# Kernel tuning notes

Measured on AMD Instinct MI355X. Metric: run time of the kernel, lower is better.

Reference implementation:

```python
import jax, jax.numpy as jnp
import numpy as np

N_NODES = 100000
N_EDGES = 300000
D = 256
N_LAYERS = 4
BN_EPS = 1e-5


def setup_inputs() -> dict:
    key = jax.random.key(0)
    ks = jax.random.split(key, 6)
    x = jax.random.normal(ks[0], (N_NODES, D), dtype=jnp.float32)
    rows = jax.random.randint(ks[1], (N_EDGES,), 0, N_NODES)
    cols = jax.random.randint(ks[2], (N_EDGES,), 0, N_NODES)
    vals = jax.random.uniform(ks[3], (N_EDGES,), dtype=jnp.float32)
    stdv = 1.0 / np.sqrt(D).astype(np.float32)
    weights = jax.random.uniform(ks[4], (N_LAYERS, D, D), jnp.float32, -stdv, stdv)
    self_weights = jax.random.uniform(ks[5], (N_LAYERS, D, D), jnp.float32, -stdv, stdv)
    gammas = jnp.ones((N_LAYERS, D), jnp.float32)
    betas = jnp.zeros((N_LAYERS, D), jnp.float32)
    return {"x": x, "vals": vals, "weights": weights, "self_weights": self_weights,
            "gammas": gammas, "betas": betas, "rows": rows, "cols": cols}


def reference(x, vals, weights, self_weights, gammas, betas, rows, cols):
    n = x.shape[0]

    def gcn_layer(h, W, SW, gamma, beta):
        # support = h @ W  -> dense [N, D]
        support = h @ W
        # spmm(adj, support): out[i] = sum_{e: rows[e]==i} vals[e] * support[cols[e]]
        agg = jax.ops.segment_sum(vals[:, None] * support[cols], rows, num_segments=n)
        out = agg + h @ SW  # self-loop term (withloop=True)
        # BatchNorm1d over nodes (training-mode batch stats, biased variance)
        mean = out.mean(axis=0)
        var = out.var(axis=0)
        out = gamma * (out - mean) * jax.lax.rsqrt(var + BN_EPS) + beta
        return jax.nn.relu(out)

    h = x
    for i in range(N_LAYERS):
        h = gcn_layer(h, weights[i], self_weights[i], gammas[i], betas[i])
    # aggrmethod='concat', dense=False -> cat(final, input)
    return jnp.concatenate([h, x], axis=1)
```

## Files before the change

### kernel.cpp

```cpp
#include <hip/hip_runtime.h>
#include <hip/hip_bf16.h>
#include <stdint.h>

#define M_NODES 100000
#define NE      300000
#define D       256
#define D2      512
#define NLAYERS 4

typedef float  f32x4  __attribute__((ext_vector_type(4)));
typedef __bf16 bf16x8 __attribute__((ext_vector_type(8)));

static __device__ __forceinline__ float bf2f(uint32_t u) {
  union { uint32_t i; float f; } v; v.i = u << 16; return v.f;
}
static __device__ __forceinline__ uint32_t f2bf(float f) {
  union { float f; uint32_t i; } v; v.f = f;
  return (v.i + 0x7fffu + ((v.i >> 16) & 1u)) >> 16;
}
static __device__ __forceinline__ void gload_lds16(const void* g, void* l) {
  __builtin_amdgcn_global_load_lds((const __attribute__((address_space(1))) uint32_t*)g,
                                   (__attribute__((address_space(3))) uint32_t*)l, 16, 0, 0);
}

__global__ void hist_kernel(const int* __restrict__ rows, int* __restrict__ counts) {
  int e = blockIdx.x * 256 + threadIdx.x;
  if (e < NE) atomicAdd(&counts[rows[e]], 1);
}

__global__ void scan1_kernel(const int* __restrict__ counts, int* __restrict__ rp,
                             int* __restrict__ bsum) {
  __shared__ int sd[256];
  int tid = threadIdx.x;
  int base = blockIdx.x * 1024 + tid * 4;
  int v0 = (base + 0 < M_NODES) ? counts[base + 0] : 0;
  int v1 = (base + 1 < M_NODES) ? counts[base + 1] : 0;
  int v2 = (base + 2 < M_NODES) ? counts[base + 2] : 0;
  int v3 = (base + 3 < M_NODES) ? counts[base + 3] : 0;
  int tsum = v0 + v1 + v2 + v3;
  sd[tid] = tsum; __syncthreads();
  for (int off = 1; off < 256; off <<= 1) {
    int x = sd[tid];
    if (tid >= off) x += sd[tid - off];
    __syncthreads(); sd[tid] = x; __syncthreads();
  }
  int excl = sd[tid] - tsum;
  if (base + 0 < M_NODES) rp[base + 0] = excl; excl += v0;
  if (base + 1 < M_NODES) rp[base + 1] = excl; excl += v1;
  if (base + 2 < M_NODES) rp[base + 2] = excl; excl += v2;
  if (base + 3 < M_NODES) rp[base + 3] = excl;
  if (tid == 255) bsum[blockIdx.x] = sd[255];
}

__global__ void scan2_kernel(const int* __restrict__ bsum, int* __restrict__ boff) {
  __shared__ int sd[128];
  int tid = threadIdx.x;
  int v = (tid < 98) ? bsum[tid] : 0;
  sd[tid] = v; __syncthreads();
  for (int off = 1; off < 128; off <<= 1) {
    int x = sd[tid];
    if (tid >= off) x += sd[tid - off];
    __syncthreads(); sd[tid] = x; __syncthreads();
  }
  if (tid < 98) boff[tid] = sd[tid] - v;
}

__global__ void scan3_kernel(int* __restrict__ rp, const int* __restrict__ boff,
                             int* __restrict__ cursor) {
  int i = blockIdx.x * 256 + threadIdx.x;
  if (i > M_NODES) return;
  int v = (i < M_NODES) ? rp[i] + boff[i >> 10] : NE;
  rp[i] = v;
  if (i < M_NODES) cursor[i] = v;
}

__global__ void scatter_kernel(const int* __restrict__ rows, const int* __restrict__ cols,
                               const float* __restrict__ vals, int* __restrict__ cursor,
                               int* __restrict__ e_col, float* __restrict__ e_val) {
  int e = blockIdx.x * 256 + threadIdx.x;
  if (e >= NE) return;
  int r = rows[e];
  int p = atomicAdd(&cursor[r], 1);
  e_col[p] = cols[e];
  e_val[p] = vals[e];
}

__global__ void prep_x_kernel(const float* __restrict__ x, ushort* __restrict__ h,
                              float* __restrict__ out) {
  size_t idx = (size_t)blockIdx.x * 256 + threadIdx.x;
  size_t i = idx >> 6; int c = (int)(idx & 63) * 4;
  float4 v = *(const float4*)(x + i * D + c);
  *(float4*)(out + i * D2 + D + c) = v;
  ushort4 o;
  o.x = (ushort)f2bf(v.x); o.y = (ushort)f2bf(v.y);
  o.z = (ushort)f2bf(v.z); o.w = (ushort)f2bf(v.w);
  *(ushort4*)(h + i * D + c) = o;
}

__global__ void conv_w_kernel(const float* __restrict__ W, const float* __restrict__ SW,
                              ushort* __restrict__ Bt) {
  int idx = blockIdx.x * 256 + threadIdx.x;
  if (idx >= NLAYERS * D2 * D) return;
  int k = idx & (D - 1);
  int n = (idx >> 8) & (D2 - 1);
  int layer = idx >> 17;
  float v = (n < D) ? W[(size_t)layer * D * D + k * D + n]
                    : SW[(size_t)layer * D * D + k * D + (n - D)];
  Bt[idx] = (ushort)f2bf(v);
}

#define BM 128
#define BN 128
#define BK 64

__global__ __launch_bounds__(256, 2)
void gemm_kernel(const ushort* __restrict__ h, const ushort* __restrict__ Bt,
                 ushort* __restrict__ outAB) {
  __shared__ __align__(16) ushort As[BM * BK];
  __shared__ __align__(16) ushort Bs[BN * BK];
  const int tid = threadIdx.x;
  const int m0 = blockIdx.x * BM;
  const int n0 = blockIdx.y * BN;
  const int wv = tid >> 6, l = tid & 63;
  const int wr = wv >> 1, wc = wv & 1;
  const int lrow = l & 15, lhi = l >> 4;

  f32x4 acc[4][4] = {};

  const int arow = tid >> 3;
  const int acb  = (tid & 7) << 4;

#pragma unroll
  for (int s = 0; s < 4; ++s) {
    const int k0 = s * BK;
#pragma unroll
    for (int p = 0; p < 4; ++p) {
      int row = p * 32 + arow;
      int grow = m0 + row; if (grow >= M_NODES) grow = M_NODES - 1;
      int gcb = acb ^ ((row & 7) << 4);
      gload_lds16(h + (size_t)grow * D + k0 + (gcb >> 1), As + row * BK + (acb >> 1));
    }
#pragma unroll
    for (int p = 0; p < 4; ++p) {
      int row = p * 32 + arow;
      int gn = n0 + row;
      int gcb = acb ^ ((row & 7) << 4);
      gload_lds16(Bt + (size_t)gn * D + k0 + (gcb >> 1), Bs + row * BK + (acb >> 1));
    }
    __syncthreads();
#pragma unroll
    for (int kk = 0; kk < 2; ++kk) {
      bf16x8 af[4], bfr[4];
#pragma unroll
      for (int mi = 0; mi < 4; ++mi) {
        int row = wr * 64 + mi * 16 + lrow;
        int off = row * 128 + ((kk * 64 + lhi * 16) ^ ((row & 7) << 4));
        af[mi] = *(const bf16x8*)((const char*)As + off);
      }
#pragma unroll
      for (int nj = 0; nj < 4; ++nj) {
        int row = wc * 64 + nj * 16 + lrow;
        int off = row * 128 + ((kk * 64 + lhi * 16) ^ ((row & 7) << 4));
        bfr[nj] = *(const bf16x8*)((const char*)Bs + off);
      }
#pragma unroll
      for (int mi = 0; mi < 4; ++mi)
#pragma unroll
        for (int nj = 0; nj < 4; ++nj)
          acc[mi][nj] = __builtin_amdgcn_mfma_f32_16x16x32_bf16(af[mi], bfr[nj], acc[mi][nj], 0, 0, 0);
    }
    __syncthreads();
  }

#pragma unroll
  for (int mi = 0; mi < 4; ++mi) {
#pragma unroll
    for (int nj = 0; nj < 4; ++nj) {
      int gc = n0 + wc * 64 + nj * 16 + lrow;
#pragma unroll
      for (int r = 0; r < 4; ++r) {
        int grow = m0 + wr * 64 + mi * 16 + lhi * 4 + r;
        if (grow < M_NODES)
          outAB[(size_t)grow * D2 + gc] = (ushort)f2bf(acc[mi][nj][r]);
      }
    }
  }
}

#define SPMM_CHUNK 16

__global__ __launch_bounds__(256, 4)
void spmm_kernel(ushort* __restrict__ AB, const int* __restrict__ rp,
                 const int* __restrict__ e_col, const float* __restrict__ e_val,
                 float* __restrict__ stats) {
  __shared__ float sstats[2 * D];
  for (int i = threadIdx.x; i < 2 * D; i += 256) sstats[i] = 0.f;
  __syncthreads();

  const int wv = threadIdx.x >> 6, l = threadIdx.x & 63;
  const int hl = l >> 5, lc = l & 31;
  const int wave = blockIdx.x * 4 + wv;
  const int row0 = wave * SPMM_CHUNK;

  float s[8] = {}, q[8] = {};

  if (row0 < M_NODES) {
    int myrp = (l <= SPMM_CHUNK) ? rp[row0 + l] : 0;
    const int ebase = __shfl(myrp, 0);
    const int ecnt  = __shfl(myrp, SPMM_CHUNK) - ebase;
    int   myc0 = (l < ecnt)      ? e_col[ebase + l]      : 0;
    float myv0 = (l < ecnt)      ? e_val[ebase + l]      : 0.f;
    int   myc1 = (64 + l < ecnt) ? e_col[ebase + 64 + l] : 0;
    float myv1 = (64 + l < ecnt) ? e_val[ebase + 64 + l] : 0.f;

    for (int t = 0; t < SPMM_CHUNK; t += 2) {
      const int i = row0 + t + hl;
      const int eA0 = __shfl(myrp, t);
      const int eA1 = __shfl(myrp, t + 1);
      const int eB1 = __shfl(myrp, t + 2);
      const int d0 = eA1 - eA0, d1 = eB1 - eA1;
      const int e0  = hl ? eA1 : eA0;
      const int deg = hl ? d1  : d0;
      const int degmax = (d0 > d1) ? d0 : d1;

      float a[8] = {};

      for (int b = 0; b < degmax; b += 4) {
        float vv[4]; uint4 sp[4];
#pragma unroll
        for (int j = 0; j < 4; ++j) {
          int ej = b + j;
          int ecl = (ej < deg) ? ej : ((deg > 0) ? deg - 1 : 0);
          int slot = e0 - ebase + ecl;
          int sl = slot & 63;
          int cA = __shfl(myc0, sl);
          int cB = __shfl(myc1, sl);
          float vA = __shfl(myv0, sl);
          float vB = __shfl(myv1, sl);
          int   c = (slot < 64) ? cA : cB;
          float v = (slot < 64) ? vA : vB;
          if (slot >= 128 && ej < deg) {
            c = e_col[e0 + ecl]; v = e_val[e0 + ecl];
          }
          vv[j] = (ej < deg) ? v : 0.f;
          sp[j] = *(const uint4*)(AB + (size_t)c * D2 + lc * 8);
        }
#pragma unroll
        for (int j = 0; j < 4; ++j) {
          a[0] += vv[j] * bf2f(sp[j].x & 0xffff);
          a[1] += vv[j] * bf2f(sp[j].x >> 16);
          a[2] += vv[j] * bf2f(sp[j].y & 0xffff);
          a[3] += vv[j] * bf2f(sp[j].y >> 16);
          a[4] += vv[j] * bf2f(sp[j].z & 0xffff);
          a[5] += vv[j] * bf2f(sp[j].z >> 16);
          a[6] += vv[j] * bf2f(sp[j].w & 0xffff);
          a[7] += vv[j] * bf2f(sp[j].w >> 16);
        }
      }

      const uint4 st = *(const uint4*)(AB + (size_t)i * D2 + D + lc * 8);
      a[0] += bf2f(st.x & 0xffff); a[1] += bf2f(st.x >> 16);
      a[2] += bf2f(st.y & 0xffff); a[3] += bf2f(st.y >> 16);
      a[4] += bf2f(st.z & 0xffff); a[5] += bf2f(st.z >> 16);
      a[6] += bf2f(st.w & 0xffff); a[7] += bf2f(st.w >> 16);

      uint4 o;
      o.x = f2bf(a[0]) | (f2bf(a[1]) << 16);
      o.y = f2bf(a[2]) | (f2bf(a[3]) << 16);
      o.z = f2bf(a[4]) | (f2bf(a[5]) << 16);
      o.w = f2bf(a[6]) | (f2bf(a[7]) << 16);
      *(uint4*)(AB + (size_t)i * D2 + D + lc * 8) = o;

#pragma unroll
      for (int k = 0; k < 8; ++k) { s[k] += a[k]; q[k] += a[k] * a[k]; }
    }
  }

  const int c0 = lc * 8;
#pragma unroll
  for (int k = 0; k < 8; ++k) {
    atomicAdd(&sstats[c0 + k], s[k]);
    atomicAdd(&sstats[D + c0 + k], q[k]);
  }
  __syncthreads();
  atomicAdd(&stats[threadIdx.x], sstats[threadIdx.x]);
  atomicAdd(&stats[D + threadIdx.x], sstats[D + threadIdx.x]);
}

template<bool LAST>
__global__ void norm_kernel(const ushort* __restrict__ AB, const float* __restrict__ stats,
                            const float* __restrict__ gamma, const float* __restrict__ beta,
                            ushort* __restrict__ hout, float* __restrict__ out) {
  const int cs = threadIdx.x & 31;
  const int rr = threadIdx.x >> 5;
  const int c0 = cs * 8;

  float sc[8], sh[8];
#pragma unroll
  for (int k = 0; k < 8; ++k) {
    float mean = stats[c0 + k] * (1.0f / M_NODES);
    float var  = stats[D + c0 + k] * (1.0f / M_NODES) - mean * mean;
    float rstd = rsqrtf(var + 1e-5f);
    float g = gamma[c0 + k];
    sc[k] = g * rstd;
    sh[k] = beta[c0 + k] - mean * sc[k];
  }

  const int r0 = blockIdx.x * 64;
#pragma unroll
  for (int rb = 0; rb < 8; ++rb) {
    int r = r0 + rb * 8 + rr;
    if (r >= M_NODES) break;
    const uint4 u = *(const uint4*)(AB + (size_t)r * D2 + D + c0);
    float f[8];
    f[0] = bf2f(u.x & 0xffff); f[1] = bf2f(u.x >> 16);
    f[2] = bf2f(u.y & 0xffff); f[3] = bf2f(u.y >> 16);
    f[4] = bf2f(u.z & 0xffff); f[5] = bf2f(u.z >> 16);
    f[6] = bf2f(u.w & 0xffff); f[7] = bf2f(u.w >> 16);
#pragma unroll
    for (int k = 0; k < 8; ++k) f[k] = fmaxf(f[k] * sc[k] + sh[k], 0.f);
    if (LAST) {
      float4 r0v = { f[0], f[1], f[2], f[3] };
      float4 r1v = { f[4], f[5], f[6], f[7] };
      *(float4*)(out + (size_t)r * D2 + c0) = r0v;
      *(float4*)(out + (size_t)r * D2 + c0 + 4) = r1v;
    } else {
      uint4 o;
      o.x = f2bf(f[0]) | (f2bf(f[1]) << 16);
      o.y = f2bf(f[2]) | (f2bf(f[3]) << 16);
      o.z = f2bf(f[4]) | (f2bf(f[5]) << 16);
      o.w = f2bf(f[6]) | (f2bf(f[7]) << 16);
      *(uint4*)(hout + (size_t)r * D + c0) = o;
    }
  }
}

extern "C" void kernel_launch(void* const* d_in, const int* in_sizes, int n_in,
                              void* d_out, int out_size, void* d_ws, size_t ws_size,
                              hipStream_t stream) {
  const float* x      = (const float*)d_in[0];
  const float* vals   = (const float*)d_in[1];
  const float* W      = (const float*)d_in[2];
  const float* SW     = (const float*)d_in[3];
  const float* gammas = (const float*)d_in[4];
  const float* betas  = (const float*)d_in[5];
  const int*   rows   = (const int*)d_in[6];
  const int*   cols   = (const int*)d_in[7];
  float* out = (float*)d_out;

  char* ws = (char*)d_ws;
  size_t off = 0;
  auto alloc = [&](size_t bytes) {
    void* p = ws + off;
    off = (off + bytes + 255) & ~(size_t)255;
    return p;
  };
  ushort* h    = (ushort*)alloc((size_t)M_NODES * D * 2);
  ushort* AB   = (ushort*)alloc((size_t)M_NODES * D2 * 2);
  ushort* Bt   = (ushort*)alloc((size_t)NLAYERS * D2 * D * 2);
  int*   rp    = (int*)alloc((M_NODES + 1) * 4);
  int*   cursor= (int*)alloc((M_NODES + 1) * 4);
  int*   e_col = (int*)alloc(NE * 4);
  float* e_val = (float*)alloc(NE * 4);
  int*   bsum  = (int*)alloc(512);
  int*   boff  = (int*)alloc(512);
  float* stats = (float*)alloc(NLAYERS * 2 * D * 4);

  hipMemsetAsync(cursor, 0, (size_t)M_NODES * 4, stream);
  hipMemsetAsync(stats, 0, (size_t)NLAYERS * 2 * D * 4, stream);

  hist_kernel<<<(NE + 255) / 256, 256, 0, stream>>>(rows, cursor);
  scan1_kernel<<<98, 256, 0, stream>>>(cursor, rp, bsum);
  scan2_kernel<<<1, 128, 0, stream>>>(bsum, boff);
  scan3_kernel<<<(M_NODES + 256) / 256, 256, 0, stream>>>(rp, boff, cursor);
  scatter_kernel<<<(NE + 255) / 256, 256, 0, stream>>>(rows, cols, vals, cursor, e_col, e_val);

  prep_x_kernel<<<(M_NODES * D / 4) / 256, 256, 0, stream>>>(x, h, out);
  conv_w_kernel<<<(NLAYERS * D2 * D) / 256, 256, 0, stream>>>(W, SW, Bt);

  const int spmm_blocks = (M_NODES + SPMM_CHUNK * 4 - 1) / (SPMM_CHUNK * 4);
  const int norm_blocks = (M_NODES + 63) / 64;
  for (int lyr = 0; lyr < NLAYERS; ++lyr) {
    gemm_kernel<<<dim3((M_NODES + BM - 1) / BM, D2 / BN), 256, 0, stream>>>(
        h, Bt + (size_t)lyr * D2 * D, AB);
    spmm_kernel<<<spmm_blocks, 256, 0, stream>>>(AB, rp, e_col, e_val,
                                                 stats + (size_t)lyr * 2 * D);
    if (lyr < NLAYERS - 1)
      norm_kernel<false><<<norm_blocks, 256, 0, stream>>>(
          AB, stats + (size_t)lyr * 2 * D, gammas + lyr * D, betas + lyr * D, h, nullptr);
    else
      norm_kernel<true><<<norm_blocks, 256, 0, stream>>>(
          AB, stats + (size_t)lyr * 2 * D, gammas + lyr * D, betas + lyr * D, nullptr, out);
  }
}
```

Before: 717.5 us.

## Stage SpMM edge metadata in LDS, widen gather unroll, two-stage stats reduction

Each wave now stages up to 256 edges' column/value pairs in shared memory instead of holding them in registers and broadcasting with shuffles; edges beyond 256 fall back to global loads. The neighbor-gather loop is unrolled to 8 loads in flight instead of 4. Per-block BN statistics are written to a partial buffer and summed by a separate small reduce kernel rather than with global atomics. The changes aim to cut shuffle overhead, raise memory-level parallelism and remove atomic contention, at the cost of extra LDS use (possibly lower occupancy), one more kernel launch per layer and more wasted gather lanes on low-degree rows.

```diff
diff --git a/kernel.cpp b/kernel.cpp
--- a/kernel.cpp
+++ b/kernel.cpp
@@ -7,6 +7,9 @@
 #define D       256
 #define D2      512
 #define NLAYERS 4
+
+#define SPMM_CHUNK  16
+#define SPMM_BLOCKS ((M_NODES + SPMM_CHUNK * 4 - 1) / (SPMM_CHUNK * 4))
 
 typedef float  f32x4  __attribute__((ext_vector_type(4)));
 typedef __bf16 bf16x8 __attribute__((ext_vector_type(8)));
@@ -187,32 +190,38 @@
   }
 }
 
-#define SPMM_CHUNK 16
-
 __global__ __launch_bounds__(256, 4)
 void spmm_kernel(ushort* __restrict__ AB, const int* __restrict__ rp,
                  const int* __restrict__ e_col, const float* __restrict__ e_val,
-                 float* __restrict__ stats) {
+                 float* __restrict__ partial) {
   __shared__ float sstats[2 * D];
+  __shared__ uint2 emeta[4][256];
   for (int i = threadIdx.x; i < 2 * D; i += 256) sstats[i] = 0.f;
-  __syncthreads();
 
   const int wv = threadIdx.x >> 6, l = threadIdx.x & 63;
   const int hl = l >> 5, lc = l & 31;
-  const int wave = blockIdx.x * 4 + wv;
-  const int row0 = wave * SPMM_CHUNK;
+  const int row0 = (blockIdx.x * 4 + wv) * SPMM_CHUNK;
+  const bool active = row0 < M_NODES;
+
+  int myrp = 0, ebase = 0, ecnt = 0;
+  if (active) {
+    myrp = (l <= SPMM_CHUNK) ? rp[row0 + l] : 0;
+    ebase = __shfl(myrp, 0);
+    ecnt  = __shfl(myrp, SPMM_CHUNK) - ebase;
+    for (int e = l; e < 256; e += 64) {
+      uint2 m = {0u, 0u};
+      if (e < ecnt) {
+        m.x = (uint32_t)e_col[ebase + e];
+        m.y = __float_as_uint(e_val[ebase + e]);
+      }
+      emeta[wv][e] = m;
+    }
+  }
+  __syncthreads();
 
   float s[8] = {}, q[8] = {};
 
-  if (row0 < M_NODES) {
-    int myrp = (l <= SPMM_CHUNK) ? rp[row0 + l] : 0;
-    const int ebase = __shfl(myrp, 0);
-    const int ecnt  = __shfl(myrp, SPMM_CHUNK) - ebase;
-    int   myc0 = (l < ecnt)      ? e_col[ebase + l]      : 0;
-    float myv0 = (l < ecnt)      ? e_val[ebase + l]      : 0.f;
-    int   myc1 = (64 + l < ecnt) ? e_col[ebase + 64 + l] : 0;
-    float myv1 = (64 + l < ecnt) ? e_val[ebase + 64 + l] : 0.f;
-
+  if (active) {
     for (int t = 0; t < SPMM_CHUNK; t += 2) {
       const int i = row0 + t + hl;
       const int eA0 = __shfl(myrp, t);
@@ -225,28 +234,25 @@
 
       float a[8] = {};
 
-      for (int b = 0; b < degmax; b += 4) {
-        float vv[4]; uint4 sp[4];
-#pragma unroll
-        for (int j = 0; j < 4; ++j) {
+      for (int b = 0; b < degmax; b += 8) {
+        float vv[8]; uint4 sp[8];
+#pragma unroll
+        for (int j = 0; j < 8; ++j) {
           int ej = b + j;
           int ecl = (ej < deg) ? ej : ((deg > 0) ? deg - 1 : 0);
           int slot = e0 - ebase + ecl;
-          int sl = slot & 63;
-          int cA = __shfl(myc0, sl);
-          int cB = __shfl(myc1, sl);
-          float vA = __shfl(myv0, sl);
-          float vB = __shfl(myv1, sl);
-          int   c = (slot < 64) ? cA : cB;
-          float v = (slot < 64) ? vA : vB;
-          if (slot >= 128 && ej < deg) {
+          int c; float v;
+          if (slot < 256) {
+            uint2 m = emeta[wv][slot];
+            c = (int)m.x; v = __uint_as_float(m.y);
+          } else {
             c = e_col[e0 + ecl]; v = e_val[e0 + ecl];
           }
           vv[j] = (ej < deg) ? v : 0.f;
           sp[j] = *(const uint4*)(AB + (size_t)c * D2 + lc * 8);
         }
 #pragma unroll
-        for (int j = 0; j < 4; ++j) {
+        for (int j = 0; j < 8; ++j) {
           a[0] += vv[j] * bf2f(sp[j].x & 0xffff);
           a[1] += vv[j] * bf2f(sp[j].x >> 16);
           a[2] += vv[j] * bf2f(sp[j].y & 0xffff);
@@ -283,8 +289,20 @@
     atomicAdd(&sstats[D + c0 + k], q[k]);
   }
   __syncthreads();
-  atomicAdd(&stats[threadIdx.x], sstats[threadIdx.x]);
-  atomicAdd(&stats[D + threadIdx.x], sstats[D + threadIdx.x]);
+  partial[(size_t)blockIdx.x * 2 * D + threadIdx.x]     = sstats[threadIdx.x];
+  partial[(size_t)blockIdx.x * 2 * D + D + threadIdx.x] = sstats[D + threadIdx.x];
+}
+
+__global__ void reduce_stats_kernel(const float* __restrict__ partial,
+                                    float* __restrict__ stats) {
+  const int t = threadIdx.x;
+  float rs = 0.f, rq = 0.f;
+  for (int b = blockIdx.x; b < SPMM_BLOCKS; b += 64) {
+    rs += partial[(size_t)b * 2 * D + t];
+    rq += partial[(size_t)b * 2 * D + D + t];
+  }
+  atomicAdd(&stats[t], rs);
+  atomicAdd(&stats[D + t], rq);
 }
 
 template<bool LAST>
@@ -355,16 +373,17 @@
     off = (off + bytes + 255) & ~(size_t)255;
     return p;
   };
-  ushort* h    = (ushort*)alloc((size_t)M_NODES * D * 2);
-  ushort* AB   = (ushort*)alloc((size_t)M_NODES * D2 * 2);
-  ushort* Bt   = (ushort*)alloc((size_t)NLAYERS * D2 * D * 2);
-  int*   rp    = (int*)alloc((M_NODES + 1) * 4);
-  int*   cursor= (int*)alloc((M_NODES + 1) * 4);
-  int*   e_col = (int*)alloc(NE * 4);
-  float* e_val = (float*)alloc(NE * 4);
-  int*   bsum  = (int*)alloc(512);
-  int*   boff  = (int*)alloc(512);
-  float* stats = (float*)alloc(NLAYERS * 2 * D * 4);
+  ushort* h      = (ushort*)alloc((size_t)M_NODES * D * 2);
+  ushort* AB     = (ushort*)alloc((size_t)M_NODES * D2 * 2);
+  ushort* Bt     = (ushort*)alloc((size_t)NLAYERS * D2 * D * 2);
+  int*   rp      = (int*)alloc((M_NODES + 1) * 4);
+  int*   cursor  = (int*)alloc((M_NODES + 1) * 4);
+  int*   e_col   = (int*)alloc(NE * 4);
+  float* e_val   = (float*)alloc(NE * 4);
+  int*   bsum    = (int*)alloc(512);
+  int*   boff    = (int*)alloc(512);
+  float* stats   = (float*)alloc(NLAYERS * 2 * D * 4);
+  float* partial = (float*)alloc((size_t)SPMM_BLOCKS * 2 * D * 4);
 
   hipMemsetAsync(cursor, 0, (size_t)M_NODES * 4, stream);
   hipMemsetAsync(stats, 0, (size_t)NLAYERS * 2 * D * 4, stream);
@@ -378,13 +397,12 @@
   prep_x_kernel<<<(M_NODES * D / 4) / 256, 256, 0, stream>>>(x, h, out);
   conv_w_kernel<<<(NLAYERS * D2 * D) / 256, 256, 0, stream>>>(W, SW, Bt);
 
-  const int spmm_blocks = (M_NODES + SPMM_CHUNK * 4 - 1) / (SPMM_CHUNK * 4);
   const int norm_blocks = (M_NODES + 63) / 64;
   for (int lyr = 0; lyr < NLAYERS; ++lyr) {
     gemm_kernel<<<dim3((M_NODES + BM - 1) / BM, D2 / BN), 256, 0, stream>>>(
         h, Bt + (size_t)lyr * D2 * D, AB);
-    spmm_kernel<<<spmm_blocks, 256, 0, stream>>>(AB, rp, e_col, e_val,
-                                                 stats + (size_t)lyr * 2 * D);
+    spmm_kernel<<<SPMM_BLOCKS, 256, 0, stream>>>(AB, rp, e_col, e_val, partial);
+    reduce_stats_kernel<<<64, 256, 0, stream>>>(partial, stats + (size_t)lyr * 2 * D);
     if (lyr < NLAYERS - 1)
       norm_kernel<false><<<norm_blocks, 256, 0, stream>>>(
           AB, stats + (size_t)lyr * 2 * D, gammas + lyr * D, betas + lyr * D, h, nullptr);
```

After: 771.2 us. 1.07x slower.

## Restructure SpMM to one row pair per wave with packed edge metadata

Applied to the files above, without the earlier changes.

The SpMM kernel now gives each wave a single pair of rows, using 1024-thread blocks, instead of a 16-row chunk processed serially. This spreads the work across many more waves and exposes more parallel gather loads. Edge column and value are packed into one uint2 array, so a single 8-byte load replaces two separate loads. Column statistics are reduced across the two half-waves with a shuffle before the shared atomics. In exchange there are more blocks and more global atomics per row, and the grid assumes M_NODES divides evenly by 32.

```diff
diff --git a/kernel.cpp b/kernel.cpp
--- a/kernel.cpp
+++ b/kernel.cpp
@@ -7,6 +7,9 @@
 #define D       256
 #define D2      512
 #define NLAYERS 4
+
+#define SPMM_TPB  1024
+#define SPMM_GRID (M_NODES / (2 * (SPMM_TPB / 64)))
 
 typedef float  f32x4  __attribute__((ext_vector_type(4)));
 typedef __bf16 bf16x8 __attribute__((ext_vector_type(8)));
@@ -76,13 +79,13 @@
 
 __global__ void scatter_kernel(const int* __restrict__ rows, const int* __restrict__ cols,
                                const float* __restrict__ vals, int* __restrict__ cursor,
-                               int* __restrict__ e_col, float* __restrict__ e_val) {
+                               uint2* __restrict__ emeta) {
   int e = blockIdx.x * 256 + threadIdx.x;
   if (e >= NE) return;
   int r = rows[e];
   int p = atomicAdd(&cursor[r], 1);
-  e_col[p] = cols[e];
-  e_val[p] = vals[e];
+  uint2 m; m.x = (uint32_t)cols[e]; m.y = __float_as_uint(vals[e]);
+  emeta[p] = m;
 }
 
 __global__ void prep_x_kernel(const float* __restrict__ x, ushort* __restrict__ h,
@@ -187,104 +190,90 @@
   }
 }
 
-#define SPMM_CHUNK 16
-
-__global__ __launch_bounds__(256, 4)
+__global__ __launch_bounds__(SPMM_TPB)
 void spmm_kernel(ushort* __restrict__ AB, const int* __restrict__ rp,
-                 const int* __restrict__ e_col, const float* __restrict__ e_val,
-                 float* __restrict__ stats) {
+                 const uint2* __restrict__ emeta, float* __restrict__ stats) {
   __shared__ float sstats[2 * D];
-  for (int i = threadIdx.x; i < 2 * D; i += 256) sstats[i] = 0.f;
+  for (int i = threadIdx.x; i < 2 * D; i += SPMM_TPB) sstats[i] = 0.f;
   __syncthreads();
 
-  const int wv = threadIdx.x >> 6, l = threadIdx.x & 63;
+  const int l  = threadIdx.x & 63;
+  const int wv = threadIdx.x >> 6;
   const int hl = l >> 5, lc = l & 31;
-  const int wave = blockIdx.x * 4 + wv;
-  const int row0 = wave * SPMM_CHUNK;
-
-  float s[8] = {}, q[8] = {};
-
-  if (row0 < M_NODES) {
-    int myrp = (l <= SPMM_CHUNK) ? rp[row0 + l] : 0;
-    const int ebase = __shfl(myrp, 0);
-    const int ecnt  = __shfl(myrp, SPMM_CHUNK) - ebase;
-    int   myc0 = (l < ecnt)      ? e_col[ebase + l]      : 0;
-    float myv0 = (l < ecnt)      ? e_val[ebase + l]      : 0.f;
-    int   myc1 = (64 + l < ecnt) ? e_col[ebase + 64 + l] : 0;
-    float myv1 = (64 + l < ecnt) ? e_val[ebase + 64 + l] : 0.f;
-
-    for (int t = 0; t < SPMM_CHUNK; t += 2) {
-      const int i = row0 + t + hl;
-      const int eA0 = __shfl(myrp, t);
-      const int eA1 = __shfl(myrp, t + 1);
-      const int eB1 = __shfl(myrp, t + 2);
-      const int d0 = eA1 - eA0, d1 = eB1 - eA1;
-      const int e0  = hl ? eA1 : eA0;
-      const int deg = hl ? d1  : d0;
-      const int degmax = (d0 > d1) ? d0 : d1;
-
-      float a[8] = {};
-
-      for (int b = 0; b < degmax; b += 4) {
-        float vv[4]; uint4 sp[4];
-#pragma unroll
-        for (int j = 0; j < 4; ++j) {
-          int ej = b + j;
-          int ecl = (ej < deg) ? ej : ((deg > 0) ? deg - 1 : 0);
-          int slot = e0 - ebase + ecl;
-          int sl = slot & 63;
-          int cA = __shfl(myc0, sl);
-          int cB = __shfl(myc1, sl);
-          float vA = __shfl(myv0, sl);
-          float vB = __shfl(myv1, sl);
-          int   c = (slot < 64) ? cA : cB;
-          float v = (slot < 64) ? vA : vB;
-          if (slot >= 128 && ej < deg) {
-            c = e_col[e0 + ecl]; v = e_val[e0 + ecl];
-          }
-          vv[j] = (ej < deg) ? v : 0.f;
-          sp[j] = *(const uint4*)(AB + (size_t)c * D2 + lc * 8);
-        }
-#pragma unroll
-        for (int j = 0; j < 4; ++j) {
-          a[0] += vv[j] * bf2f(sp[j].x & 0xffff);
-          a[1] += vv[j] * bf2f(sp[j].x >> 16);
-          a[2] += vv[j] * bf2f(sp[j].y & 0xffff);
-          a[3] += vv[j] * bf2f(sp[j].y >> 16);
-          a[4] += vv[j] * bf2f(sp[j].z & 0xffff);
-          a[5] += vv[j] * bf2f(sp[j].z >> 16);
-          a[6] += vv[j] * bf2f(sp[j].w & 0xffff);
-          a[7] += vv[j] * bf2f(sp[j].w >> 16);
-        }
+  const int pair = blockIdx.x * (SPMM_TPB / 64) + wv;
+  const int row  = pair * 2 + hl;
+
+  int myrp = (l < 3) ? rp[pair * 2 + l] : 0;
+  const int lo  = __shfl(myrp, 0);
+  const int mid = __shfl(myrp, 1);
+  const int end = __shfl(myrp, 2);
+  const int ebase = lo, ecnt = end - lo;
+  const int e0  = hl ? mid : lo;
+  const int d0 = mid - lo, d1 = end - mid;
+  const int deg = hl ? d1 : d0;
+  const int degmax = (d0 > d1) ? d0 : d1;
+
+  uint2 mymeta = {0u, 0u};
+  if (l < ecnt) mymeta = emeta[ebase + l];
+
+  const uint4 st = *(const uint4*)(AB + (size_t)row * D2 + D + lc * 8);
+
+  float a[8] = {};
+  for (int b = 0; b < degmax; b += 4) {
+    float vv[4]; uint4 sp[4];
+#pragma unroll
+    for (int j = 0; j < 4; ++j) {
+      int ej = b + j;
+      int ecl = (ej < deg) ? ej : ((deg > 0) ? deg - 1 : 0);
+      int slot = e0 - ebase + ecl;
+      int sl = slot & 63;
+      int c   = __shfl((int)mymeta.x, sl);
+      float v = __shfl(__uint_as_float(mymeta.y), sl);
+      if (slot >= 64 && ej < deg) {
+        uint2 m = emeta[e0 + ecl]; c = (int)m.x; v = __uint_as_float(m.y);
       }
-
-      const uint4 st = *(const uint4*)(AB + (size_t)i * D2 + D + lc * 8);
-      a[0] += bf2f(st.x & 0xffff); a[1] += bf2f(st.x >> 16);
-      a[2] += bf2f(st.y & 0xffff); a[3] += bf2f(st.y >> 16);
-      a[4] += bf2f(st.z & 0xffff); a[5] += bf2f(st.z >> 16);
-      a[6] += bf2f(st.w & 0xffff); a[7] += bf2f(st.w >> 16);
-
-      uint4 o;
-      o.x = f2bf(a[0]) | (f2bf(a[1]) << 16);
-      o.y = f2bf(a[2]) | (f2bf(a[3]) << 16);
-      o.z = f2bf(a[4]) | (f2bf(a[5]) << 16);
-      o.w = f2bf(a[6]) | (f2bf(a[7]) << 16);
-      *(uint4*)(AB + (size_t)i * D2 + D + lc * 8) = o;
-
-#pragma unroll
-      for (int k = 0; k < 8; ++k) { s[k] += a[k]; q[k] += a[k] * a[k]; }
-    }
-  }
+      vv[j] = (ej < deg) ? v : 0.f;
+      sp[j] = *(const uint4*)(AB + (size_t)c * D2 + lc * 8);
+    }
+#pragma unroll
+    for (int j = 0; j < 4; ++j) {
+      a[0] += vv[j] * bf2f(sp[j].x & 0xffff);
+      a[1] += vv[j] * bf2f(sp[j].x >> 16);
+      a[2] += vv[j] * bf2f(sp[j].y & 0xffff);
+      a[3] += vv[j] * bf2f(sp[j].y >> 16);
+      a[4] += vv[j] * bf2f(sp[j].z & 0xffff);
+      a[5] += vv[j] * bf2f(sp[j].z >> 16);
+      a[6] += vv[j] * bf2f(sp[j].w & 0xffff);
+      a[7] += vv[j] * bf2f(sp[j].w >> 16);
+    }
+  }
+
+  a[0] += bf2f(st.x & 0xffff); a[1] += bf2f(st.x >> 16);
+  a[2] += bf2f(st.y & 0xffff); a[3] += bf2f(st.y >> 16);
+  a[4] += bf2f(st.z & 0xffff); a[5] += bf2f(st.z >> 16);
+  a[6] += bf2f(st.w & 0xffff); a[7] += bf2f(st.w >> 16);
+
+  uint4 o;
+  o.x = f2bf(a[0]) | (f2bf(a[1]) << 16);
+  o.y = f2bf(a[2]) | (f2bf(a[3]) << 16);
+  o.z = f2bf(a[4]) | (f2bf(a[5]) << 16);
+  o.w = f2bf(a[6]) | (f2bf(a[7]) << 16);
+  *(uint4*)(AB + (size_t)row * D2 + D + lc * 8) = o;
 
   const int c0 = lc * 8;
 #pragma unroll
   for (int k = 0; k < 8; ++k) {
-    atomicAdd(&sstats[c0 + k], s[k]);
-    atomicAdd(&sstats[D + c0 + k], q[k]);
+    float a2 = a[k] * a[k];
+    float sk = a[k] + __shfl_xor(a[k], 32);
+    float qk = a2   + __shfl_xor(a2,   32);
+    if (hl == 0) {
+      atomicAdd(&sstats[c0 + k], sk);
+      atomicAdd(&sstats[D + c0 + k], qk);
+    }
   }
   __syncthreads();
-  atomicAdd(&stats[threadIdx.x], sstats[threadIdx.x]);
-  atomicAdd(&stats[D + threadIdx.x], sstats[D + threadIdx.x]);
+  if (threadIdx.x < 2 * D)
+    atomicAdd(&stats[threadIdx.x], sstats[threadIdx.x]);
 }
 
 template<bool LAST>
@@ -355,16 +344,15 @@
     off = (off + bytes + 255) & ~(size_t)255;
     return p;
   };
-  ushort* h    = (ushort*)alloc((size_t)M_NODES * D * 2);
-  ushort* AB   = (ushort*)alloc((size_t)M_NODES * D2 * 2);
-  ushort* Bt   = (ushort*)alloc((size_t)NLAYERS * D2 * D * 2);
-  int*   rp    = (int*)alloc((M_NODES + 1) * 4);
-  int*   cursor= (int*)alloc((M_NODES + 1) * 4);
-  int*   e_col = (int*)alloc(NE * 4);
-  float* e_val = (float*)alloc(NE * 4);
-  int*   bsum  = (int*)alloc(512);
-  int*   boff  = (int*)alloc(512);
-  float* stats = (float*)alloc(NLAYERS * 2 * D * 4);
+  ushort* h     = (ushort*)alloc((size_t)M_NODES * D * 2);
+  ushort* AB    = (ushort*)alloc((size_t)M_NODES * D2 * 2);
+  ushort* Bt    = (ushort*)alloc((size_t)NLAYERS * D2 * D * 2);
+  int*   rp     = (int*)alloc((M_NODES + 1) * 4);
+  int*   cursor = (int*)alloc((M_NODES + 1) * 4);
+  uint2* emeta  = (uint2*)alloc((size_t)NE * 8);
+  int*   bsum   = (int*)alloc(512);
+  int*   boff   = (int*)alloc(512);
+  float* stats  = (float*)alloc(NLAYERS * 2 * D * 4);
 
   hipMemsetAsync(cursor, 0, (size_t)M_NODES * 4, stream);
   hipMemsetAsync(stats, 0, (size_t)NLAYERS * 2 * D * 4, stream);
@@ -373,18 +361,17 @@
   scan1_kernel<<<98, 256, 0, stream>>>(cursor, rp, bsum);
   scan2_kernel<<<1, 128, 0, stream>>>(bsum, boff);
   scan3_kernel<<<(M_NODES + 256) / 256, 256, 0, stream>>>(rp, boff, cursor);
-  scatter_kernel<<<(NE + 255) / 256, 256, 0, stream>>>(rows, cols, vals, cursor, e_col, e_val);
+  scatter_kernel<<<(NE + 255) / 256, 256, 0, stream>>>(rows, cols, vals, cursor, emeta);
 
   prep_x_kernel<<<(M_NODES * D / 4) / 256, 256, 0, stream>>>(x, h, out);
   conv_w_kernel<<<(NLAYERS * D2 * D) / 256, 256, 0, stream>>>(W, SW, Bt);
 
-  const int spmm_blocks = (M_NODES + SPMM_CHUNK * 4 - 1) / (SPMM_CHUNK * 4);
   const int norm_blocks = (M_NODES + 63) / 64;
   for (int lyr = 0; lyr < NLAYERS; ++lyr) {
     gemm_kernel<<<dim3((M_NODES + BM - 1) / BM, D2 / BN), 256, 0, stream>>>(
         h, Bt + (size_t)lyr * D2 * D, AB);
-    spmm_kernel<<<spmm_blocks, 256, 0, stream>>>(AB, rp, e_col, e_val,
-                                                 stats + (size_t)lyr * 2 * D);
+    spmm_kernel<<<SPMM_GRID, SPMM_TPB, 0, stream>>>(AB, rp, emeta,
+                                                    stats + (size_t)lyr * 2 * D);
     if (lyr < NLAYERS - 1)
       norm_kernel<false><<<norm_blocks, 256, 0, stream>>>(
           AB, stats + (size_t)lyr * 2 * D, gammas + lyr * D, betas + lyr * D, h, nullptr);
```

Measured after the change: 1.145 ms. 59.5% more time.

## Fuse BatchNorm+ReLU into next GEMM's A-load and restructure SpMM

Applied to the files above, without the earlier changes.

Drops the per-layer norm kernel for intermediate layers. A tiny kernel now computes the BN scale and shift, and the next GEMM applies scale, shift, ReLU and the bf16 conversion while loading A tiles through registers instead of direct global-to-LDS loads. Layer 0 converts fp32 x on the fly, which removes the bf16 copy of h. SpMM now gives one row per wave with 4 columns per lane, packs col and val into one uint2 array, writes to a separate P buffer, and raises its occupancy bound. The cost is extra ALU work and register-path loads in the GEMM prologue, and the normalize work is repeated across the four N-tile blocks.

```diff
diff --git a/kernel.cpp b/kernel.cpp
--- a/kernel.cpp
+++ b/kernel.cpp
@@ -7,6 +7,8 @@
 #define D       256
 #define D2      512
 #define NLAYERS 4
+
+#define SPMM_CHUNK 16
 
 typedef float  f32x4  __attribute__((ext_vector_type(4)));
 typedef __bf16 bf16x8 __attribute__((ext_vector_type(8)));
@@ -76,25 +78,20 @@
 
 __global__ void scatter_kernel(const int* __restrict__ rows, const int* __restrict__ cols,
                                const float* __restrict__ vals, int* __restrict__ cursor,
-                               int* __restrict__ e_col, float* __restrict__ e_val) {
+                               uint2* __restrict__ emeta) {
   int e = blockIdx.x * 256 + threadIdx.x;
   if (e >= NE) return;
   int r = rows[e];
   int p = atomicAdd(&cursor[r], 1);
-  e_col[p] = cols[e];
-  e_val[p] = vals[e];
-}
-
-__global__ void prep_x_kernel(const float* __restrict__ x, ushort* __restrict__ h,
-                              float* __restrict__ out) {
+  uint2 m; m.x = (uint32_t)cols[e]; m.y = __float_as_uint(vals[e]);
+  emeta[p] = m;
+}
+
+__global__ void prep_x_kernel(const float* __restrict__ x, float* __restrict__ out) {
   size_t idx = (size_t)blockIdx.x * 256 + threadIdx.x;
   size_t i = idx >> 6; int c = (int)(idx & 63) * 4;
   float4 v = *(const float4*)(x + i * D + c);
   *(float4*)(out + i * D2 + D + c) = v;
-  ushort4 o;
-  o.x = (ushort)f2bf(v.x); o.y = (ushort)f2bf(v.y);
-  o.z = (ushort)f2bf(v.z); o.w = (ushort)f2bf(v.w);
-  *(ushort4*)(h + i * D + c) = o;
 }
 
 __global__ void conv_w_kernel(const float* __restrict__ W, const float* __restrict__ SW,
@@ -109,12 +106,25 @@
   Bt[idx] = (ushort)f2bf(v);
 }
 
+__global__ void bn_fin_kernel(const float* __restrict__ stats, const float* __restrict__ gamma,
+                              const float* __restrict__ beta, float* __restrict__ ss) {
+  int c = threadIdx.x;
+  float mean = stats[c] * (1.0f / M_NODES);
+  float var  = stats[D + c] * (1.0f / M_NODES) - mean * mean;
+  float rstd = rsqrtf(var + 1e-5f);
+  float sc = gamma[c] * rstd;
+  ss[c] = sc;
+  ss[D + c] = beta[c] - mean * sc;
+}
+
 #define BM 128
 #define BN 128
 #define BK 64
 
+template<int MODE>
 __global__ __launch_bounds__(256, 2)
-void gemm_kernel(const ushort* __restrict__ h, const ushort* __restrict__ Bt,
+void gemm_kernel(const float* __restrict__ x, const ushort* __restrict__ P,
+                 const float* __restrict__ ss, const ushort* __restrict__ Bt,
                  ushort* __restrict__ outAB) {
   __shared__ __align__(16) ushort As[BM * BK];
   __shared__ __align__(16) ushort Bs[BN * BK];
@@ -129,16 +139,45 @@
 
   const int arow = tid >> 3;
   const int acb  = (tid & 7) << 4;
+  const int acol = acb >> 1;
 
 #pragma unroll
   for (int s = 0; s < 4; ++s) {
     const int k0 = s * BK;
+    float4 sc0, sc1, sh0, sh1;
+    if (MODE == 1) {
+      sc0 = *(const float4*)(ss + k0 + acol);
+      sc1 = *(const float4*)(ss + k0 + acol + 4);
+      sh0 = *(const float4*)(ss + D + k0 + acol);
+      sh1 = *(const float4*)(ss + D + k0 + acol + 4);
+    }
 #pragma unroll
     for (int p = 0; p < 4; ++p) {
       int row = p * 32 + arow;
       int grow = m0 + row; if (grow >= M_NODES) grow = M_NODES - 1;
-      int gcb = acb ^ ((row & 7) << 4);
-      gload_lds16(h + (size_t)grow * D + k0 + (gcb >> 1), As + row * BK + (acb >> 1));
+      float f[8];
+      if (MODE == 0) {
+        float4 v0 = *(const float4*)(x + (size_t)grow * D + k0 + acol);
+        float4 v1 = *(const float4*)(x + (size_t)grow * D + k0 + acol + 4);
+        f[0] = v0.x; f[1] = v0.y; f[2] = v0.z; f[3] = v0.w;
+        f[4] = v1.x; f[5] = v1.y; f[6] = v1.z; f[7] = v1.w;
+      } else {
+        uint4 u = *(const uint4*)(P + (size_t)grow * D + k0 + acol);
+        f[0] = fmaxf(bf2f(u.x & 0xffff) * sc0.x + sh0.x, 0.f);
+        f[1] = fmaxf(bf2f(u.x >> 16)    * sc0.y + sh0.y, 0.f);
+        f[2] = fmaxf(bf2f(u.y & 0xffff) * sc0.z + sh0.z, 0.f);
+        f[3] = fmaxf(bf2f(u.y >> 16)    * sc0.w + sh0.w, 0.f);
+        f[4] = fmaxf(bf2f(u.z & 0xffff) * sc1.x + sh1.x, 0.f);
+        f[5] = fmaxf(bf2f(u.z >> 16)    * sc1.y + sh1.y, 0.f);
+        f[6] = fmaxf(bf2f(u.w & 0xffff) * sc1.z + sh1.z, 0.f);
+        f[7] = fmaxf(bf2f(u.w >> 16)    * sc1.w + sh1.w, 0.f);
+      }
+      uint4 o;
+      o.x = f2bf(f[0]) | (f2bf(f[1]) << 16);
+      o.y = f2bf(f[2]) | (f2bf(f[3]) << 16);
+      o.z = f2bf(f[4]) | (f2bf(f[5]) << 16);
+      o.w = f2bf(f[6]) | (f2bf(f[7]) << 16);
+      *(uint4*)((char*)As + row * 128 + (acb ^ ((row & 7) << 4))) = o;
     }
 #pragma unroll
     for (int p = 0; p < 4; ++p) {
@@ -187,110 +226,87 @@
   }
 }
 
-#define SPMM_CHUNK 16
-
-__global__ __launch_bounds__(256, 4)
-void spmm_kernel(ushort* __restrict__ AB, const int* __restrict__ rp,
-                 const int* __restrict__ e_col, const float* __restrict__ e_val,
+__global__ __launch_bounds__(256, 8)
+void spmm_kernel(const ushort* __restrict__ AB, ushort* __restrict__ P,
+                 const int* __restrict__ rp, const uint2* __restrict__ emeta,
                  float* __restrict__ stats) {
   __shared__ float sstats[2 * D];
   for (int i = threadIdx.x; i < 2 * D; i += 256) sstats[i] = 0.f;
   __syncthreads();
 
   const int wv = threadIdx.x >> 6, l = threadIdx.x & 63;
-  const int hl = l >> 5, lc = l & 31;
   const int wave = blockIdx.x * 4 + wv;
   const int row0 = wave * SPMM_CHUNK;
 
-  float s[8] = {}, q[8] = {};
+  float s0 = 0, s1 = 0, s2 = 0, s3 = 0, q0 = 0, q1 = 0, q2 = 0, q3 = 0;
 
   if (row0 < M_NODES) {
-    int myrp = (l <= SPMM_CHUNK) ? rp[row0 + l] : 0;
+    const int nrows = (M_NODES - row0 < SPMM_CHUNK) ? (M_NODES - row0) : SPMM_CHUNK;
+    int myrp = (l <= nrows) ? rp[row0 + l] : 0;
     const int ebase = __shfl(myrp, 0);
-    const int ecnt  = __shfl(myrp, SPMM_CHUNK) - ebase;
-    int   myc0 = (l < ecnt)      ? e_col[ebase + l]      : 0;
-    float myv0 = (l < ecnt)      ? e_val[ebase + l]      : 0.f;
-    int   myc1 = (64 + l < ecnt) ? e_col[ebase + 64 + l] : 0;
-    float myv1 = (64 + l < ecnt) ? e_val[ebase + 64 + l] : 0.f;
-
-    for (int t = 0; t < SPMM_CHUNK; t += 2) {
-      const int i = row0 + t + hl;
-      const int eA0 = __shfl(myrp, t);
-      const int eA1 = __shfl(myrp, t + 1);
-      const int eB1 = __shfl(myrp, t + 2);
-      const int d0 = eA1 - eA0, d1 = eB1 - eA1;
-      const int e0  = hl ? eA1 : eA0;
-      const int deg = hl ? d1  : d0;
-      const int degmax = (d0 > d1) ? d0 : d1;
-
-      float a[8] = {};
-
-      for (int b = 0; b < degmax; b += 4) {
-        float vv[4]; uint4 sp[4];
+    const int ecnt  = __shfl(myrp, nrows) - ebase;
+    uint2 m0 = {0u, 0u}, m1 = {0u, 0u};
+    if (l < ecnt)      m0 = emeta[ebase + l];
+    if (64 + l < ecnt) m1 = emeta[ebase + 64 + l];
+
+    for (int t = 0; t < nrows; ++t) {
+      const int i = row0 + t;
+      const int e0 = __shfl(myrp, t);
+      const int e1 = __shfl(myrp, t + 1);
+      const int deg = e1 - e0;
+
+      const ushort4 st = *(const ushort4*)(AB + (size_t)i * D2 + D + 4 * l);
+      float a0 = bf2f(st.x), a1 = bf2f(st.y), a2 = bf2f(st.z), a3 = bf2f(st.w);
+
+      for (int b = 0; b < deg; b += 4) {
+        float vv[4]; ushort4 sp[4];
 #pragma unroll
         for (int j = 0; j < 4; ++j) {
           int ej = b + j;
-          int ecl = (ej < deg) ? ej : ((deg > 0) ? deg - 1 : 0);
+          int ecl = (ej < deg) ? ej : (deg - 1);
           int slot = e0 - ebase + ecl;
           int sl = slot & 63;
-          int cA = __shfl(myc0, sl);
-          int cB = __shfl(myc1, sl);
-          float vA = __shfl(myv0, sl);
-          float vB = __shfl(myv1, sl);
+          int cA = __shfl((int)m0.x, sl);
+          int cB = __shfl((int)m1.x, sl);
+          float vA = __shfl(__uint_as_float(m0.y), sl);
+          float vB = __shfl(__uint_as_float(m1.y), sl);
           int   c = (slot < 64) ? cA : cB;
           float v = (slot < 64) ? vA : vB;
           if (slot >= 128 && ej < deg) {
-            c = e_col[e0 + ecl]; v = e_val[e0 + ecl];
+            uint2 m = emeta[e0 + ecl]; c = (int)m.x; v = __uint_as_float(m.y);
           }
           vv[j] = (ej < deg) ? v : 0.f;
-          sp[j] = *(const uint4*)(AB + (size_t)c * D2 + lc * 8);
+          sp[j] = *(const ushort4*)(AB + (size_t)c * D2 + 4 * l);
         }
 #pragma unroll
         for (int j = 0; j < 4; ++j) {
-          a[0] += vv[j] * bf2f(sp[j].x & 0xffff);
-          a[1] += vv[j] * bf2f(sp[j].x >> 16);
-          a[2] += vv[j] * bf2f(sp[j].y & 0xffff);
-          a[3] += vv[j] * bf2f(sp[j].y >> 16);
-          a[4] += vv[j] * bf2f(sp[j].z & 0xffff);
-          a[5] += vv[j] * bf2f(sp[j].z >> 16);
-          a[6] += vv[j] * bf2f(sp[j].w & 0xffff);
-          a[7] += vv[j] * bf2f(sp[j].w >> 16);
+          a0 += vv[j] * bf2f(sp[j].x); a1 += vv[j] * bf2f(sp[j].y);
+          a2 += vv[j] * bf2f(sp[j].z); a3 += vv[j] * bf2f(sp[j].w);
         }
       }
 
-      const uint4 st = *(const uint4*)(AB + (size_t)i * D2 + D + lc * 8);
-      a[0] += bf2f(st.x & 0xffff); a[1] += bf2f(st.x >> 16);
-      a[2] += bf2f(st.y & 0xffff); a[3] += bf2f(st.y >> 16);
-      a[4] += bf2f(st.z & 0xffff); a[5] += bf2f(st.z >> 16);
-      a[6] += bf2f(st.w & 0xffff); a[7] += bf2f(st.w >> 16);
-
-      uint4 o;
-      o.x = f2bf(a[0]) | (f2bf(a[1]) << 16);
-      o.y = f2bf(a[2]) | (f2bf(a[3]) << 16);
-      o.z = f2bf(a[4]) | (f2bf(a[5]) << 16);
-      o.w = f2bf(a[6]) | (f2bf(a[7]) << 16);
-      *(uint4*)(AB + (size_t)i * D2 + D + lc * 8) = o;
-
-#pragma unroll
-      for (int k = 0; k < 8; ++k) { s[k] += a[k]; q[k] += a[k] * a[k]; }
-    }
-  }
-
-  const int c0 = lc * 8;
-#pragma unroll
-  for (int k = 0; k < 8; ++k) {
-    atomicAdd(&sstats[c0 + k], s[k]);
-    atomicAdd(&sstats[D + c0 + k], q[k]);
-  }
+      ushort4 o;
+      o.x = (ushort)f2bf(a0); o.y = (ushort)f2bf(a1);
+      o.z = (ushort)f2bf(a2); o.w = (ushort)f2bf(a3);
+      *(ushort4*)(P + (size_t)i * D + 4 * l) = o;
+      s0 += a0; q0 += a0 * a0; s1 += a1; q1 += a1 * a1;
+      s2 += a2; q2 += a2 * a2; s3 += a3; q3 += a3 * a3;
+    }
+  }
+
+  const int c0 = 4 * l;
+  atomicAdd(&sstats[c0 + 0], s0); atomicAdd(&sstats[c0 + 1], s1);
+  atomicAdd(&sstats[c0 + 2], s2); atomicAdd(&sstats[c0 + 3], s3);
+  atomicAdd(&sstats[D + c0 + 0], q0); atomicAdd(&sstats[D + c0 + 1], q1);
+  atomicAdd(&sstats[D + c0 + 2], q2); atomicAdd(&sstats[D + c0 + 3], q3);
   __syncthreads();
   atomicAdd(&stats[threadIdx.x], sstats[threadIdx.x]);
   atomicAdd(&stats[D + threadIdx.x], sstats[D + threadIdx.x]);
 }
 
-template<bool LAST>
-__global__ void norm_kernel(const ushort* __restrict__ AB, const float* __restrict__ stats,
-                            const float* __restrict__ gamma, const float* __restrict__ beta,
-                            ushort* __restrict__ hout, float* __restrict__ out) {
+__global__ void norm_last_kernel(const ushort* __restrict__ P, const float* __restrict__ stats,
+                                 const float* __restrict__ gamma, const float* __restrict__ beta,
+                                 float* __restrict__ out) {
   const int cs = threadIdx.x & 31;
   const int rr = threadIdx.x >> 5;
   const int c0 = cs * 8;
@@ -311,7 +327,7 @@
   for (int rb = 0; rb < 8; ++rb) {
     int r = r0 + rb * 8 + rr;
     if (r >= M_NODES) break;
-    const uint4 u = *(const uint4*)(AB + (size_t)r * D2 + D + c0);
+    const uint4 u = *(const uint4*)(P + (size_t)r * D + c0);
     float f[8];
     f[0] = bf2f(u.x & 0xffff); f[1] = bf2f(u.x >> 16);
     f[2] = bf2f(u.y & 0xffff); f[3] = bf2f(u.y >> 16);
@@ -319,19 +335,10 @@
     f[6] = bf2f(u.w & 0xffff); f[7] = bf2f(u.w >> 16);
 #pragma unroll
     for (int k = 0; k < 8; ++k) f[k] = fmaxf(f[k] * sc[k] + sh[k], 0.f);
-    if (LAST) {
-      float4 r0v = { f[0], f[1], f[2], f[3] };
-      float4 r1v = { f[4], f[5], f[6], f[7] };
-      *(float4*)(out + (size_t)r * D2 + c0) = r0v;
-      *(float4*)(out + (size_t)r * D2 + c0 + 4) = r1v;
-    } else {
-      uint4 o;
-      o.x = f2bf(f[0]) | (f2bf(f[1]) << 16);
-      o.y = f2bf(f[2]) | (f2bf(f[3]) << 16);
-      o.z = f2bf(f[4]) | (f2bf(f[5]) << 16);
-      o.w = f2bf(f[6]) | (f2bf(f[7]) << 16);
-      *(uint4*)(hout + (size_t)r * D + c0) = o;
-    }
+    float4 r0v = { f[0], f[1], f[2], f[3] };
+    float4 r1v = { f[4], f[5], f[6], f[7] };
+    *(float4*)(out + (size_t)r * D2 + c0) = r0v;
+    *(float4*)(out + (size_t)r * D2 + c0 + 4) = r1v;
   }
 }
 
@@ -355,16 +362,16 @@
     off = (off + bytes + 255) & ~(size_t)255;
     return p;
   };
-  ushort* h    = (ushort*)alloc((size_t)M_NODES * D * 2);
-  ushort* AB   = (ushort*)alloc((size_t)M_NODES * D2 * 2);
-  ushort* Bt   = (ushort*)alloc((size_t)NLAYERS * D2 * D * 2);
-  int*   rp    = (int*)alloc((M_NODES + 1) * 4);
-  int*   cursor= (int*)alloc((M_NODES + 1) * 4);
-  int*   e_col = (int*)alloc(NE * 4);
-  float* e_val = (float*)alloc(NE * 4);
-  int*   bsum  = (int*)alloc(512);
-  int*   boff  = (int*)alloc(512);
-  float* stats = (float*)alloc(NLAYERS * 2 * D * 4);
+  ushort* AB     = (ushort*)alloc((size_t)M_NODES * D2 * 2);
+  ushort* P      = (ushort*)alloc((size_t)M_NODES * D * 2);
+  ushort* Bt     = (ushort*)alloc((size_t)NLAYERS * D2 * D * 2);
+  int*    rp     = (int*)alloc((M_NODES + 1) * 4);
+  int*    cursor = (int*)alloc((M_NODES + 1) * 4);
+  uint2*  emeta  = (uint2*)alloc((size_t)NE * 8);
+  int*    bsum   = (int*)alloc(512);
+  int*    boff   = (int*)alloc(512);
+  float*  stats  = (float*)alloc(NLAYERS * 2 * D * 4);
+  float*  ss     = (float*)alloc(2 * D * 4);
 
   hipMemsetAsync(cursor, 0, (size_t)M_NODES * 4, stream);
   hipMemsetAsync(stats, 0, (size_t)NLAYERS * 2 * D * 4, stream);
@@ -373,23 +380,27 @@
   scan1_kernel<<<98, 256, 0, stream>>>(cursor, rp, bsum);
   scan2_kernel<<<1, 128, 0, stream>>>(bsum, boff);
   scan3_kernel<<<(M_NODES + 256) / 256, 256, 0, stream>>>(rp, boff, cursor);
-  scatter_kernel<<<(NE + 255) / 256, 256, 0, stream>>>(rows, cols, vals, cursor, e_col, e_val);
-
-  prep_x_kernel<<<(M_NODES * D / 4) / 256, 256, 0, stream>>>(x, h, out);
+  scatter_kernel<<<(NE + 255) / 256, 256, 0, stream>>>(rows, cols, vals, cursor, emeta);
+
+  prep_x_kernel<<<(M_NODES * D / 4) / 256, 256, 0, stream>>>(x, out);
   conv_w_kernel<<<(NLAYERS * D2 * D) / 256, 256, 0, stream>>>(W, SW, Bt);
 
+  const dim3 ggrid((M_NODES + BM - 1) / BM, D2 / BN);
   const int spmm_blocks = (M_NODES + SPMM_CHUNK * 4 - 1) / (SPMM_CHUNK * 4);
-  const int norm_blocks = (M_NODES + 63) / 64;
   for (int lyr = 0; lyr < NLAYERS; ++lyr) {
-    gemm_kernel<<<dim3((M_NODES + BM - 1) / BM, D2 / BN), 256, 0, stream>>>(
-        h, Bt + (size_t)lyr * D2 * D, AB);
-    spmm_kernel<<<spmm_blocks, 256, 0, stream>>>(AB, rp, e_col, e_val,
+    if (lyr == 0)
+      gemm_kernel<0><<<ggrid, 256, 0, stream>>>(x, nullptr, nullptr,
+                                                Bt + (size_t)lyr * D2 * D, AB);
+    else
+      gemm_kernel<1><<<ggrid, 256, 0, stream>>>(nullptr, P, ss,
+                                                Bt + (size_t)lyr * D2 * D, AB);
+    spmm_kernel<<<spmm_blocks, 256, 0, stream>>>(AB, P, rp, emeta,
                                                  stats + (size_t)lyr * 2 * D);
     if (lyr < NLAYERS - 1)
-      norm_kernel<false><<<norm_blocks, 256, 0, stream>>>(
-          AB, stats + (size_t)lyr * 2 * D, gammas + lyr * D, betas + lyr * D, h, nullptr);
+      bn_fin_kernel<<<1, 256, 0, stream>>>(stats + (size_t)lyr * 2 * D,
+                                           gammas + lyr * D, betas + lyr * D, ss);
     else
-      norm_kernel<true><<<norm_blocks, 256, 0, stream>>>(
-          AB, stats + (size_t)lyr * 2 * D, gammas + lyr * D, betas + lyr * D, nullptr, out);
-  }
-}
+      norm_last_kernel<<<(M_NODES + 63) / 64, 256, 0, stream>>>(
+          P, stats + (size_t)lyr * 2 * D, gammas + lyr * D, betas + lyr * D, out);
+  }
+}
```

After: 712.0 us. About the same (-0.8%).
